# Kernel tuning notes

Measured on AMD Instinct MI355X. Metric: run time of the kernel, lower is better.

## Reference

```python
import jax, jax.numpy as jnp
import numpy as np

B, L, H, D = 2, 2048, 16, 64
E = H * D  # 1024

def setup_inputs() -> dict:
    key = jax.random.key(0)
    k1, k2, k3 = jax.random.split(key, 3)
    net_in = jax.random.normal(k1, (B, L, E), dtype=jnp.float32)
    # torch nn.Linear weights are [out_features, in_features]; scale like kaiming-uniform-ish
    W_qkv = jax.random.normal(k2, (3 * E, E), dtype=jnp.float32) * (1.0 / np.sqrt(E))
    W_out = jax.random.normal(k3, (E, E), dtype=jnp.float32) * (1.0 / np.sqrt(E))
    return {"net_in": net_in, "W_qkv": W_qkv, "W_out": W_out}

def reference(net_in, W_qkv, W_out):
    b, l, c = net_in.shape
    h, d = H, D
    # c_proj: x @ W_qkv.T -> (B, L, 3E), split into q, k, v
    qkv = jnp.einsum('blc,ec->ble', net_in, W_qkv)
    q, k, v = jnp.split(qkv, 3, axis=-1)
    # reshape to (B, H, L, D)
    q = q.reshape(b, l, h, d).transpose(0, 2, 1, 3)
    k = k.reshape(b, l, h, d).transpose(0, 2, 1, 3)
    v = v.reshape(b, l, h, d).transpose(0, 2, 1, 3)
    scale = 1.0 / np.sqrt(d).astype(np.float32)
    attn = jnp.einsum('bhqd,bhkd->bhqk', q, k) * scale  # (B, H, L, L)
    causal = jnp.tril(jnp.ones((l, l), dtype=bool))
    attn = jnp.where(causal[None, None, :, :], attn, -jnp.inf)
    attn = jax.nn.softmax(attn, axis=-1)
    out = jnp.einsum('bhqk,bhkd->bhqd', attn, v)  # (B, H, L, D)
    out = out.transpose(0, 2, 1, 3).reshape(b, l, c)
    return jnp.einsum('blc,ec->ble', out, W_out)
```

## Files before the change

### kernel.cpp

```cpp
#include <hip/hip_runtime.h>
#include <hip/hip_bf16.h>

#define LOG2E 1.44269504088896340736f

typedef __attribute__((ext_vector_type(8))) short s16x8;
typedef __attribute__((ext_vector_type(4))) short s16x4;
typedef __attribute__((ext_vector_type(2))) unsigned int u32x2;
typedef __attribute__((ext_vector_type(4))) float f32x4;

__device__ inline short f2bf(float f) {
  __hip_bfloat16 h = __float2bfloat16(f);
  union { __hip_bfloat16 h; short s; } u; u.h = h; return u.s;
}

__device__ inline void gl_lds16(const void* g, void* l) {
  __builtin_amdgcn_global_load_lds(
      (const __attribute__((address_space(1))) void*)g,
      (__attribute__((address_space(3))) void*)l, 16, 0, 0);
}

__global__ __launch_bounds__(256)
void cvt_all(const float* __restrict__ Wqkv, const float* __restrict__ Wout,
             const float* __restrict__ net,
             short* __restrict__ dWqkv, short* __restrict__ dWout,
             short* __restrict__ dnet) {
  int bid = blockIdx.x;
  const float* src; short* dst; int i;
  if (bid < 3072)      { src = Wqkv; dst = dWqkv; i = bid * 256 + threadIdx.x; }
  else if (bid < 4096) { src = Wout; dst = dWout; i = (bid - 3072) * 256 + threadIdx.x; }
  else                 { src = net;  dst = dnet;  i = (bid - 4096) * 256 + threadIdx.x; }
  f32x4 v = ((const f32x4*)src)[i];
  s16x4 o;
  o[0] = f2bf(v[0]); o[1] = f2bf(v[1]); o[2] = f2bf(v[2]); o[3] = f2bf(v[3]);
  ((s16x4*)dst)[i] = o;
}

template<int OUTF32, int VTRANS>
__global__ __launch_bounds__(256)
void gemm128(const short* __restrict__ A, int lda,
             const short* __restrict__ B,
             void* __restrict__ Cp, int ldc, int K) {
  int m0 = blockIdx.x * 128;
  int n0 = blockIdx.y * 128;
  int t = threadIdx.x;
  int w = t >> 6, lane = t & 63;
  int l16 = lane & 15, quad = lane >> 4;
  int wm = w >> 1, wn = w & 1;

  __shared__ __align__(16) short Bs[128 * 32];
  __shared__ __align__(16) short As[128 * 32];

  int scell = ((t & 3) ^ ((t >> 3) & 3)) * 8;
  const short* bsrc = B + (size_t)(n0 + (t >> 2)) * K + scell;
  const short* asrc = A + (size_t)(m0 + (t >> 2)) * lda + scell;
  int rcell = (quad ^ ((l16 >> 1) & 3)) * 8;

  f32x4 acc[4][4];
#pragma unroll
  for (int i = 0; i < 4; ++i)
#pragma unroll
    for (int j = 0; j < 4; ++j) acc[i][j] = (f32x4){0.f, 0.f, 0.f, 0.f};

  for (int k0 = 0; k0 < K; k0 += 32) {
    __syncthreads();
#pragma unroll
    for (int r = 0; r < 2; ++r)
      gl_lds16(asrc + k0 + (size_t)r * 64 * lda, (char*)As + r * 4096 + w * 1024);
#pragma unroll
    for (int r = 0; r < 2; ++r)
      gl_lds16(bsrc + k0 + (size_t)r * 64 * K, (char*)Bs + r * 4096 + w * 1024);
    __syncthreads();

    s16x8 af[4], bf[4];
#pragma unroll
    for (int i = 0; i < 4; ++i) {
      af[i] = *(const s16x8*)(As + (wm * 64 + i * 16 + l16) * 32 + rcell);
      bf[i] = *(const s16x8*)(Bs + (wn * 64 + i * 16 + l16) * 32 + rcell);
    }
#pragma unroll
    for (int i = 0; i < 4; ++i)
#pragma unroll
      for (int j = 0; j < 4; ++j)
        acc[i][j] = __builtin_amdgcn_mfma_f32_16x16x32_bf16(af[i], bf[j], acc[i][j], 0, 0, 0);
  }

  if (VTRANS && n0 >= 2048) {
    short* Cs = (short*)Cp;
#pragma unroll
    for (int i = 0; i < 4; ++i)
#pragma unroll
      for (int j = 0; j < 4; ++j) {
        int colg = n0 + wn * 64 + j * 16 + l16;
        int d = colg & 63;
        size_t dst = (size_t)(m0 + wm * 64 + d) * ldc + (colg - d) + i * 16 + quad * 4;
        s16x4 ob;
#pragma unroll
        for (int rr = 0; rr < 4; ++rr) ob[rr] = f2bf(acc[i][j][rr]);
        *(s16x4*)(Cs + dst) = ob;
      }
  } else {
#pragma unroll
    for (int i = 0; i < 4; ++i)
#pragma unroll
      for (int j = 0; j < 4; ++j)
#pragma unroll
        for (int rr = 0; rr < 4; ++rr) {
          size_t row = m0 + wm * 64 + i * 16 + quad * 4 + rr;
          size_t col = n0 + wn * 64 + j * 16 + l16;
          if (OUTF32) ((float*)Cp)[row * ldc + col] = acc[i][j][rr];
          else        ((short*)Cp)[row * ldc + col] = f2bf(acc[i][j][rr]);
        }
  }
}

__global__ __launch_bounds__(256)
void attn(short* __restrict__ qkv) {
  const int L = 2048, E3 = 3072, EO = 1024;
  int id = (int)(blockIdx.x + (blockIdx.y << 5));
  int xcd = id & 7;
  int s = id >> 3;
  int bh = xcd * 4 + (s & 3);
  int u = s >> 2;
  int vv = u & 15;
  int qidx = (u & 16) ? (31 - vv) : vv;
  int b = bh >> 4, h = bh & 15;
  int q0 = qidx * 64;
  int t = threadIdx.x;
  int wave = t >> 6, lane = t & 63;
  int l16 = lane & 15, quad = lane >> 4;
  int qw = q0 + wave * 16;
  const float SENT = -3.0e38f;
  const float SC = 0.125f * LOG2E;

  __shared__ __align__(16) short Ks[2][2][64][32];
  __shared__ __align__(16) short Vt[2][2][64][32];
  __shared__ __align__(16) short Pw[4][16 * 64];

  int rowbase = b * L;
  const short* qp = qkv + (size_t)(rowbase + qw + l16) * E3 + h * 64 + quad * 8;
  s16x8 qf[2];
#pragma unroll
  for (int c = 0; c < 2; ++c) {
    s16x8 raw = *(const s16x8*)(qp + c * 32);
#pragma unroll
    for (int j = 0; j < 8; ++j) {
      union { float f; int i; } u2; u2.i = ((int)(unsigned short)raw[j]) << 16;
      raw[j] = f2bf(u2.f * SC);
    }
    qf[c] = raw;
  }

  int scell = ((lane & 3) ^ ((lane >> 3) & 3)) * 8;
  const short* ksrc = qkv + (size_t)(rowbase + wave * 16 + (lane >> 2)) * E3 + EO
                      + h * 64 + scell;
  const short* vsrc = qkv + (size_t)(rowbase + wave * 16 + (lane >> 2)) * E3 + 2 * EO
                      + h * 64 + scell;
  int rcell = (quad ^ ((l16 >> 1) & 3)) * 8;
  int pbase = l16 * 64, pxor = l16 & 7;

  float l_acc = 0.f;
  f32x4 o[4];
#pragma unroll
  for (int j = 0; j < 4; ++j) o[j] = (f32x4){0.f, 0.f, 0.f, 0.f};

  int nkb = qidx + 1;

  gl_lds16(ksrc,      (char*)Ks + wave * 1024);
  gl_lds16(ksrc + 32, (char*)Ks + 4096 + wave * 1024);
  gl_lds16(vsrc,      (char*)Vt + wave * 1024);
  gl_lds16(vsrc + 32, (char*)Vt + 4096 + wave * 1024);

  for (int kb = 0; kb < nkb; ++kb) {
    int cur = kb & 1;
    __syncthreads();
    if (kb + 1 < nkb) {
      size_t koff = (size_t)((kb + 1) * 64) * E3;
      int nb = cur ^ 1;
      gl_lds16(ksrc + koff,      (char*)Ks + nb * 8192 + wave * 1024);
      gl_lds16(ksrc + koff + 32, (char*)Ks + nb * 8192 + 4096 + wave * 1024);
      gl_lds16(vsrc + koff,      (char*)Vt + nb * 8192 + wave * 1024);
      gl_lds16(vsrc + koff + 32, (char*)Vt + nb * 8192 + 4096 + wave * 1024);
    }

    int mtile = (qw - kb * 64) >> 4;

    f32x4 sf[4];
#pragma unroll
    for (int st = 0; st < 4; ++st) {
      if (st <= mtile) {
        s16x8 kf0 = *(const s16x8*)(&Ks[cur][0][st * 16 + l16][0] + rcell);
        s16x8 kf1 = *(const s16x8*)(&Ks[cur][1][st * 16 + l16][0] + rcell);
        f32x4 tt = (f32x4){0.f, 0.f, 0.f, 0.f};
        tt = __builtin_amdgcn_mfma_f32_16x16x32_bf16(kf0, qf[0], tt, 0, 0, 0);
        tt = __builtin_amdgcn_mfma_f32_16x16x32_bf16(kf1, qf[1], tt, 0, 0, 0);
        sf[st] = tt;
      }
    }
    if (mtile < 4) {
#pragma unroll
      for (int st = 0; st < 4; ++st) {
        if (st == mtile) {
#pragma unroll
          for (int r = 0; r < 4; ++r)
            if (quad * 4 + r > l16) sf[st][r] = SENT;
        } else if (st > mtile) {
          sf[st] = (f32x4){SENT, SENT, SENT, SENT};
        }
      }
    }

#pragma unroll
    for (int st = 0; st < 4; ++st)
#pragma unroll
      for (int r = 0; r < 4; ++r) {
        float p = __builtin_amdgcn_exp2f(sf[st][r]);
        sf[st][r] = p;
        l_acc += p;
      }

#pragma unroll
    for (int st = 0; st < 4; ++st) {
      unsigned u0 = __float_as_uint(sf[st][0]) + 0x8000u;
      unsigned u1 = __float_as_uint(sf[st][1]) + 0x8000u;
      unsigned u2 = __float_as_uint(sf[st][2]) + 0x8000u;
      unsigned u3 = __float_as_uint(sf[st][3]) + 0x8000u;
      u32x2 d;
      d[0] = __builtin_amdgcn_perm(u1, u0, 0x07060302u);
      d[1] = __builtin_amdgcn_perm(u3, u2, 0x07060302u);
      int cw = (st * 2 + (quad >> 1)) ^ pxor;
      *(u32x2*)(&Pw[wave][pbase + cw * 8 + (quad & 1) * 4]) = d;
    }
    asm volatile("s_waitcnt lgkmcnt(0)" ::: "memory");
#pragma unroll
    for (int kc = 0; kc < 2; ++kc) {
      s16x8 pf = *(const s16x8*)(&Pw[wave][pbase + (((kc * 4 + quad) ^ pxor) * 8)]);
#pragma unroll
      for (int j = 0; j < 4; ++j) {
        s16x8 vf = *(const s16x8*)(&Vt[cur][kc][j * 16 + l16][0] + rcell);
        o[j] = __builtin_amdgcn_mfma_f32_16x16x32_bf16(vf, pf, o[j], 0, 0, 0);
      }
    }
  }

  l_acc += __shfl_xor(l_acc, 16);
  l_acc += __shfl_xor(l_acc, 32);
  float inv = 1.f / l_acc;
  size_t obase = (size_t)(rowbase + qw + l16) * E3 + h * 64;
#pragma unroll
  for (int j = 0; j < 4; ++j) {
    s16x4 ob;
#pragma unroll
    for (int r = 0; r < 4; ++r) ob[r] = f2bf(o[j][r] * inv);
    *(s16x4*)(qkv + obase + j * 16 + quad * 4) = ob;
  }
}

extern "C" void kernel_launch(void* const* d_in, const int* in_sizes, int n_in,
                              void* d_out, int out_size, void* d_ws, size_t ws_size,
                              hipStream_t stream) {
  const float* net_in = (const float*)d_in[0];
  const float* W_qkv  = (const float*)d_in[1];
  const float* W_out  = (const float*)d_in[2];

  short* Wqkvb = (short*)d_ws;
  short* Woutb = Wqkvb + (size_t)3072 * 1024;
  short* qkv   = Woutb + (size_t)1024 * 1024;
  short* netb  = (short*)d_out;

  cvt_all<<<8192, 256, 0, stream>>>(W_qkv, W_out, net_in, Wqkvb, Woutb, netb);

  gemm128<0, 1><<<dim3(32, 24), 256, 0, stream>>>(netb, 1024, Wqkvb, qkv, 3072, 1024);
  attn<<<dim3(32, 32), 256, 0, stream>>>(qkv);
  gemm128<1, 0><<<dim3(32, 8), 256, 0, stream>>>(qkv, 3072, Woutb, d_out, 1024, 1024);
}
```

Measured before the change: 185.8 us.

## Process two 64-row query tiles per attention block to reuse K/V loads

Each attention workgroup now handles 128 query rows, as two groups of 16 rows per wave, instead of 64. Every K/V tile staged in LDS therefore feeds twice as many MFMAs, and the grid is halved. The query-pair mapping is changed so causal work stays balanced. The cost is more registers (two accumulator sets, launch bounds of 256 with 2 blocks), fewer blocks to fill the CUs, and some wasted masked work on the first tile's diagonal blocks.

```diff
diff --git a/kernel.cpp b/kernel.cpp
--- a/kernel.cpp
+++ b/kernel.cpp
@@ -113,7 +113,7 @@
   }
 }
 
-__global__ __launch_bounds__(256)
+__global__ __launch_bounds__(256, 2)
 void attn(short* __restrict__ qkv) {
   const int L = 2048, E3 = 3072, EO = 1024;
   int id = (int)(blockIdx.x + (blockIdx.y << 5));
@@ -121,33 +121,36 @@
   int s = id >> 3;
   int bh = xcd * 4 + (s & 3);
   int u = s >> 2;
-  int vv = u & 15;
-  int qidx = (u & 16) ? (31 - vv) : vv;
+  int qp = (u < 8) ? u : 23 - u;
   int b = bh >> 4, h = bh & 15;
-  int q0 = qidx * 64;
+  int q0 = qp * 128;
   int t = threadIdx.x;
   int wave = t >> 6, lane = t & 63;
   int l16 = lane & 15, quad = lane >> 4;
-  int qw = q0 + wave * 16;
+  int qw0 = q0 + wave * 16;
+  int qw1 = qw0 + 64;
   const float SENT = -3.0e38f;
   const float SC = 0.125f * LOG2E;
 
   __shared__ __align__(16) short Ks[2][2][64][32];
   __shared__ __align__(16) short Vt[2][2][64][32];
-  __shared__ __align__(16) short Pw[4][16 * 64];
+  __shared__ __align__(16) short Pw[4][2][16 * 64];
 
   int rowbase = b * L;
-  const short* qp = qkv + (size_t)(rowbase + qw + l16) * E3 + h * 64 + quad * 8;
-  s16x8 qf[2];
-#pragma unroll
-  for (int c = 0; c < 2; ++c) {
-    s16x8 raw = *(const s16x8*)(qp + c * 32);
-#pragma unroll
-    for (int j = 0; j < 8; ++j) {
-      union { float f; int i; } u2; u2.i = ((int)(unsigned short)raw[j]) << 16;
-      raw[j] = f2bf(u2.f * SC);
-    }
-    qf[c] = raw;
+  s16x8 qf[2][2];
+#pragma unroll
+  for (int g = 0; g < 2; ++g) {
+    const short* qp_ptr = qkv + (size_t)(rowbase + qw0 + g * 64 + l16) * E3 + h * 64 + quad * 8;
+#pragma unroll
+    for (int c = 0; c < 2; ++c) {
+      s16x8 raw = *(const s16x8*)(qp_ptr + c * 32);
+#pragma unroll
+      for (int j = 0; j < 8; ++j) {
+        union { float f; int i; } u2; u2.i = ((int)(unsigned short)raw[j]) << 16;
+        raw[j] = f2bf(u2.f * SC);
+      }
+      qf[g][c] = raw;
+    }
   }
 
   int scell = ((lane & 3) ^ ((lane >> 3) & 3)) * 8;
@@ -158,12 +161,12 @@
   int rcell = (quad ^ ((l16 >> 1) & 3)) * 8;
   int pbase = l16 * 64, pxor = l16 & 7;
 
-  float l_acc = 0.f;
-  f32x4 o[4];
-#pragma unroll
-  for (int j = 0; j < 4; ++j) o[j] = (f32x4){0.f, 0.f, 0.f, 0.f};
-
-  int nkb = qidx + 1;
+  float l0 = 0.f, l1 = 0.f;
+  f32x4 o0[4], o1[4];
+#pragma unroll
+  for (int j = 0; j < 4; ++j) { o0[j] = (f32x4){0.f,0.f,0.f,0.f}; o1[j] = (f32x4){0.f,0.f,0.f,0.f}; }
+
+  int nkb = 2 * qp + 2;
 
   gl_lds16(ksrc,      (char*)Ks + wave * 1024);
   gl_lds16(ksrc + 32, (char*)Ks + 4096 + wave * 1024);
@@ -182,76 +185,117 @@
       gl_lds16(vsrc + koff + 32, (char*)Vt + nb * 8192 + 4096 + wave * 1024);
     }
 
-    int mtile = (qw - kb * 64) >> 4;
-
-    f32x4 sf[4];
+    int mt0 = (qw0 - kb * 64) >> 4;
+    int mt1 = mt0 + 4;
+
+    f32x4 sf0[4], sf1[4];
 #pragma unroll
     for (int st = 0; st < 4; ++st) {
-      if (st <= mtile) {
+      if (st <= mt1) {
         s16x8 kf0 = *(const s16x8*)(&Ks[cur][0][st * 16 + l16][0] + rcell);
         s16x8 kf1 = *(const s16x8*)(&Ks[cur][1][st * 16 + l16][0] + rcell);
+        if (st <= mt0) {
+          f32x4 tt = (f32x4){0.f, 0.f, 0.f, 0.f};
+          tt = __builtin_amdgcn_mfma_f32_16x16x32_bf16(kf0, qf[0][0], tt, 0, 0, 0);
+          tt = __builtin_amdgcn_mfma_f32_16x16x32_bf16(kf1, qf[0][1], tt, 0, 0, 0);
+          sf0[st] = tt;
+        }
         f32x4 tt = (f32x4){0.f, 0.f, 0.f, 0.f};
-        tt = __builtin_amdgcn_mfma_f32_16x16x32_bf16(kf0, qf[0], tt, 0, 0, 0);
-        tt = __builtin_amdgcn_mfma_f32_16x16x32_bf16(kf1, qf[1], tt, 0, 0, 0);
-        sf[st] = tt;
-      }
-    }
-    if (mtile < 4) {
+        tt = __builtin_amdgcn_mfma_f32_16x16x32_bf16(kf0, qf[1][0], tt, 0, 0, 0);
+        tt = __builtin_amdgcn_mfma_f32_16x16x32_bf16(kf1, qf[1][1], tt, 0, 0, 0);
+        sf1[st] = tt;
+      }
+    }
+    if (mt0 < 4) {
 #pragma unroll
       for (int st = 0; st < 4; ++st) {
-        if (st == mtile) {
+        if (st == mt0) {
 #pragma unroll
           for (int r = 0; r < 4; ++r)
-            if (quad * 4 + r > l16) sf[st][r] = SENT;
-        } else if (st > mtile) {
-          sf[st] = (f32x4){SENT, SENT, SENT, SENT};
+            if (quad * 4 + r > l16) sf0[st][r] = SENT;
+        } else if (st > mt0) {
+          sf0[st] = (f32x4){SENT, SENT, SENT, SENT};
         }
       }
     }
+    if (mt1 < 4) {
+#pragma unroll
+      for (int st = 0; st < 4; ++st) {
+        if (st == mt1) {
+#pragma unroll
+          for (int r = 0; r < 4; ++r)
+            if (quad * 4 + r > l16) sf1[st][r] = SENT;
+        } else if (st > mt1) {
+          sf1[st] = (f32x4){SENT, SENT, SENT, SENT};
+        }
+      }
+    }
 
 #pragma unroll
     for (int st = 0; st < 4; ++st)
 #pragma unroll
       for (int r = 0; r < 4; ++r) {
-        float p = __builtin_amdgcn_exp2f(sf[st][r]);
-        sf[st][r] = p;
-        l_acc += p;
+        float p0 = __builtin_amdgcn_exp2f(sf0[st][r]);
+        sf0[st][r] = p0; l0 += p0;
+        float p1 = __builtin_amdgcn_exp2f(sf1[st][r]);
+        sf1[st][r] = p1; l1 += p1;
       }
 
 #pragma unroll
     for (int st = 0; st < 4; ++st) {
-      unsigned u0 = __float_as_uint(sf[st][0]) + 0x8000u;
-      unsigned u1 = __float_as_uint(sf[st][1]) + 0x8000u;
-      unsigned u2 = __float_as_uint(sf[st][2]) + 0x8000u;
-      unsigned u3 = __float_as_uint(sf[st][3]) + 0x8000u;
-      u32x2 d;
-      d[0] = __builtin_amdgcn_perm(u1, u0, 0x07060302u);
-      d[1] = __builtin_amdgcn_perm(u3, u2, 0x07060302u);
       int cw = (st * 2 + (quad >> 1)) ^ pxor;
-      *(u32x2*)(&Pw[wave][pbase + cw * 8 + (quad & 1) * 4]) = d;
+      {
+        unsigned a0 = __float_as_uint(sf0[st][0]) + 0x8000u;
+        unsigned a1 = __float_as_uint(sf0[st][1]) + 0x8000u;
+        unsigned a2 = __float_as_uint(sf0[st][2]) + 0x8000u;
+        unsigned a3 = __float_as_uint(sf0[st][3]) + 0x8000u;
+        u32x2 d;
+        d[0] = __builtin_amdgcn_perm(a1, a0, 0x07060302u);
+        d[1] = __builtin_amdgcn_perm(a3, a2, 0x07060302u);
+        *(u32x2*)(&Pw[wave][0][pbase + cw * 8 + (quad & 1) * 4]) = d;
+      }
+      {
+        unsigned a0 = __float_as_uint(sf1[st][0]) + 0x8000u;
+        unsigned a1 = __float_as_uint(sf1[st][1]) + 0x8000u;
+        unsigned a2 = __float_as_uint(sf1[st][2]) + 0x8000u;
+        unsigned a3 = __float_as_uint(sf1[st][3]) + 0x8000u;
+        u32x2 d;
+        d[0] = __builtin_amdgcn_perm(a1, a0, 0x07060302u);
+        d[1] = __builtin_amdgcn_perm(a3, a2, 0x07060302u);
+        *(u32x2*)(&Pw[wave][1][pbase + cw * 8 + (quad & 1) * 4]) = d;
+      }
     }
     asm volatile("s_waitcnt lgkmcnt(0)" ::: "memory");
 #pragma unroll
     for (int kc = 0; kc < 2; ++kc) {
-      s16x8 pf = *(const s16x8*)(&Pw[wave][pbase + (((kc * 4 + quad) ^ pxor) * 8)]);
+      s16x8 pf0 = *(const s16x8*)(&Pw[wave][0][pbase + (((kc * 4 + quad) ^ pxor) * 8)]);
+      s16x8 pf1 = *(const s16x8*)(&Pw[wave][1][pbase + (((kc * 4 + quad) ^ pxor) * 8)]);
 #pragma unroll
       for (int j = 0; j < 4; ++j) {
         s16x8 vf = *(const s16x8*)(&Vt[cur][kc][j * 16 + l16][0] + rcell);
-        o[j] = __builtin_amdgcn_mfma_f32_16x16x32_bf16(vf, pf, o[j], 0, 0, 0);
-      }
-    }
-  }
-
-  l_acc += __shfl_xor(l_acc, 16);
-  l_acc += __shfl_xor(l_acc, 32);
-  float inv = 1.f / l_acc;
-  size_t obase = (size_t)(rowbase + qw + l16) * E3 + h * 64;
+        o0[j] = __builtin_amdgcn_mfma_f32_16x16x32_bf16(vf, pf0, o0[j], 0, 0, 0);
+        o1[j] = __builtin_amdgcn_mfma_f32_16x16x32_bf16(vf, pf1, o1[j], 0, 0, 0);
+      }
+    }
+  }
+
+  l0 += __shfl_xor(l0, 16);
+  l0 += __shfl_xor(l0, 32);
+  l1 += __shfl_xor(l1, 16);
+  l1 += __shfl_xor(l1, 32);
+  float inv0 = 1.f / l0, inv1 = 1.f / l1;
+  size_t ob0 = (size_t)(rowbase + qw0 + l16) * E3 + h * 64;
+  size_t ob1 = (size_t)(rowbase + qw1 + l16) * E3 + h * 64;
 #pragma unroll
   for (int j = 0; j < 4; ++j) {
-    s16x4 ob;
-#pragma unroll
-    for (int r = 0; r < 4; ++r) ob[r] = f2bf(o[j][r] * inv);
-    *(s16x4*)(qkv + obase + j * 16 + quad * 4) = ob;
+    s16x4 w0, w1;
+#pragma unroll
+    for (int r = 0; r < 4; ++r) {
+      w0[r] = f2bf(o0[j][r] * inv0);
+      w1[r] = f2bf(o1[j][r] * inv1);
+    }
+    *(s16x4*)(qkv + ob0 + j * 16 + quad * 4) = w0;
+    *(s16x4*)(qkv + ob1 + j * 16 + quad * 4) = w1;
   }
 }
 
@@ -270,6 +314,6 @@
   cvt_all<<<8192, 256, 0, stream>>>(W_qkv, W_out, net_in, Wqkvb, Woutb, netb);
 
   gemm128<0, 1><<<dim3(32, 24), 256, 0, stream>>>(netb, 1024, Wqkvb, qkv, 3072, 1024);
-  attn<<<dim3(32, 32), 256, 0, stream>>>(qkv);
+  attn<<<dim3(32, 16), 256, 0, stream>>>(qkv);
   gemm128<1, 0><<<dim3(32, 8), 256, 0, stream>>>(qkv, 3072, Woutb, d_out, 1024, 1024);
 }
```

New measurement: 200.6 us. 8.0% more time.

## Switch attention to 32x32 MFMA with in-register P via permlane swap and key split

Applied to the files above, without the earlier changes.

Reworks the attention kernel to use 32x32x16 bf16 MFMAs, with waves split into 2 query halves × 2 key halves. The P tile now moves between lane halves with permlane32_swap instead of a round trip through LDS, and the two key-half partial outputs are combined through shared memory at the end. This is meant to remove the LDS traffic and waitcnt stall for P, cut the MFMA instruction count, and let fully masked key halves be skipped. The cost is a final cross-wave reduction with two barriers, and half the waves sit idle during the output write.

```diff
diff --git a/kernel.cpp b/kernel.cpp
--- a/kernel.cpp
+++ b/kernel.cpp
@@ -7,6 +7,7 @@
 typedef __attribute__((ext_vector_type(4))) short s16x4;
 typedef __attribute__((ext_vector_type(2))) unsigned int u32x2;
 typedef __attribute__((ext_vector_type(4))) float f32x4;
+typedef __attribute__((ext_vector_type(16))) float f32x16;
 
 __device__ inline short f2bf(float f) {
   __hip_bfloat16 h = __float2bfloat16(f);
@@ -113,7 +114,7 @@
   }
 }
 
-__global__ __launch_bounds__(256)
+__global__ __launch_bounds__(256, 4)
 void attn(short* __restrict__ qkv) {
   const int L = 2048, E3 = 3072, EO = 1024;
   int id = (int)(blockIdx.x + (blockIdx.y << 5));
@@ -127,27 +128,31 @@
   int q0 = qidx * 64;
   int t = threadIdx.x;
   int wave = t >> 6, lane = t & 63;
-  int l16 = lane & 15, quad = lane >> 4;
-  int qw = q0 + wave * 16;
+  int qh = wave >> 1, kh = wave & 1;
+  int l31 = lane & 31, hsel = lane >> 5;
+  int khi4 = hsel * 4;
+  int key = (lane >> 1) & 3;
   const float SENT = -3.0e38f;
   const float SC = 0.125f * LOG2E;
 
   __shared__ __align__(16) short Ks[2][2][64][32];
   __shared__ __align__(16) short Vt[2][2][64][32];
-  __shared__ __align__(16) short Pw[4][16 * 64];
 
   int rowbase = b * L;
-  const short* qp = qkv + (size_t)(rowbase + qw + l16) * E3 + h * 64 + quad * 8;
-  s16x8 qf[2];
-#pragma unroll
-  for (int c = 0; c < 2; ++c) {
-    s16x8 raw = *(const s16x8*)(qp + c * 32);
-#pragma unroll
-    for (int j = 0; j < 8; ++j) {
-      union { float f; int i; } u2; u2.i = ((int)(unsigned short)raw[j]) << 16;
-      raw[j] = f2bf(u2.f * SC);
-    }
-    qf[c] = raw;
+
+  s16x8 qf[4];
+  {
+    const short* qp = qkv + (size_t)(rowbase + q0 + qh * 32 + l31) * E3 + h * 64 + hsel * 8;
+#pragma unroll
+    for (int e = 0; e < 4; ++e) {
+      s16x8 raw = *(const s16x8*)(qp + e * 16);
+#pragma unroll
+      for (int j = 0; j < 8; ++j) {
+        union { float f; int i; } u2; u2.i = ((int)(unsigned short)raw[j]) << 16;
+        raw[j] = f2bf(u2.f * SC);
+      }
+      qf[e] = raw;
+    }
   }
 
   int scell = ((lane & 3) ^ ((lane >> 3) & 3)) * 8;
@@ -155,13 +160,10 @@
                       + h * 64 + scell;
   const short* vsrc = qkv + (size_t)(rowbase + wave * 16 + (lane >> 2)) * E3 + 2 * EO
                       + h * 64 + scell;
-  int rcell = (quad ^ ((l16 >> 1) & 3)) * 8;
-  int pbase = l16 * 64, pxor = l16 & 7;
 
   float l_acc = 0.f;
-  f32x4 o[4];
-#pragma unroll
-  for (int j = 0; j < 4; ++j) o[j] = (f32x4){0.f, 0.f, 0.f, 0.f};
+  f32x16 o0 = (f32x16){0.f,0.f,0.f,0.f,0.f,0.f,0.f,0.f,0.f,0.f,0.f,0.f,0.f,0.f,0.f,0.f};
+  f32x16 o1 = o0;
 
   int nkb = qidx + 1;
 
@@ -182,76 +184,91 @@
       gl_lds16(vsrc + koff + 32, (char*)Vt + nb * 8192 + 4096 + wave * 1024);
     }
 
-    int mtile = (qw - kb * 64) >> 4;
-
-    f32x4 sf[4];
-#pragma unroll
-    for (int st = 0; st < 4; ++st) {
-      if (st <= mtile) {
-        s16x8 kf0 = *(const s16x8*)(&Ks[cur][0][st * 16 + l16][0] + rcell);
-        s16x8 kf1 = *(const s16x8*)(&Ks[cur][1][st * 16 + l16][0] + rcell);
-        f32x4 tt = (f32x4){0.f, 0.f, 0.f, 0.f};
-        tt = __builtin_amdgcn_mfma_f32_16x16x32_bf16(kf0, qf[0], tt, 0, 0, 0);
-        tt = __builtin_amdgcn_mfma_f32_16x16x32_bf16(kf1, qf[1], tt, 0, 0, 0);
-        sf[st] = tt;
-      }
-    }
-    if (mtile < 4) {
-#pragma unroll
-      for (int st = 0; st < 4; ++st) {
-        if (st == mtile) {
-#pragma unroll
-          for (int r = 0; r < 4; ++r)
-            if (quad * 4 + r > l16) sf[st][r] = SENT;
-        } else if (st > mtile) {
-          sf[st] = (f32x4){SENT, SENT, SENT, SENT};
+    int rel = (q0 + qh * 32) - (kb * 64 + kh * 32);
+    if (rel > -32) {
+      int krow = kh * 32 + l31;
+      s16x8 kf0 = *(const s16x8*)(&Ks[cur][0][krow][((0 + hsel) ^ key) * 8]);
+      s16x8 kf1 = *(const s16x8*)(&Ks[cur][0][krow][((2 + hsel) ^ key) * 8]);
+      s16x8 kf2 = *(const s16x8*)(&Ks[cur][1][krow][((0 + hsel) ^ key) * 8]);
+      s16x8 kf3 = *(const s16x8*)(&Ks[cur][1][krow][((2 + hsel) ^ key) * 8]);
+      s16x8 vf00 = *(const s16x8*)(&Vt[cur][kh][ 0 + l31][((0 + hsel) ^ key) * 8]);
+      s16x8 vf01 = *(const s16x8*)(&Vt[cur][kh][32 + l31][((0 + hsel) ^ key) * 8]);
+      s16x8 vf10 = *(const s16x8*)(&Vt[cur][kh][ 0 + l31][((2 + hsel) ^ key) * 8]);
+      s16x8 vf11 = *(const s16x8*)(&Vt[cur][kh][32 + l31][((2 + hsel) ^ key) * 8]);
+
+      f32x16 sf = (f32x16){0.f,0.f,0.f,0.f,0.f,0.f,0.f,0.f,0.f,0.f,0.f,0.f,0.f,0.f,0.f,0.f};
+      sf = __builtin_amdgcn_mfma_f32_32x32x16_bf16(kf0, qf[0], sf, 0, 0, 0);
+      sf = __builtin_amdgcn_mfma_f32_32x32x16_bf16(kf1, qf[1], sf, 0, 0, 0);
+      sf = __builtin_amdgcn_mfma_f32_32x32x16_bf16(kf2, qf[2], sf, 0, 0, 0);
+      sf = __builtin_amdgcn_mfma_f32_32x32x16_bf16(kf3, qf[3], sf, 0, 0, 0);
+
+      if (rel < 31) {
+        int thr = rel + l31 - khi4;
+#pragma unroll
+        for (int r = 0; r < 16; ++r) {
+          const int base_k = (r & 3) + 8 * (r >> 2);
+          if (base_k > thr) sf[r] = SENT;
         }
       }
-    }
-
-#pragma unroll
-    for (int st = 0; st < 4; ++st)
-#pragma unroll
-      for (int r = 0; r < 4; ++r) {
-        float p = __builtin_amdgcn_exp2f(sf[st][r]);
-        sf[st][r] = p;
-        l_acc += p;
-      }
-
-#pragma unroll
-    for (int st = 0; st < 4; ++st) {
-      unsigned u0 = __float_as_uint(sf[st][0]) + 0x8000u;
-      unsigned u1 = __float_as_uint(sf[st][1]) + 0x8000u;
-      unsigned u2 = __float_as_uint(sf[st][2]) + 0x8000u;
-      unsigned u3 = __float_as_uint(sf[st][3]) + 0x8000u;
-      u32x2 d;
-      d[0] = __builtin_amdgcn_perm(u1, u0, 0x07060302u);
-      d[1] = __builtin_amdgcn_perm(u3, u2, 0x07060302u);
-      int cw = (st * 2 + (quad >> 1)) ^ pxor;
-      *(u32x2*)(&Pw[wave][pbase + cw * 8 + (quad & 1) * 4]) = d;
-    }
-    asm volatile("s_waitcnt lgkmcnt(0)" ::: "memory");
-#pragma unroll
-    for (int kc = 0; kc < 2; ++kc) {
-      s16x8 pf = *(const s16x8*)(&Pw[wave][pbase + (((kc * 4 + quad) ^ pxor) * 8)]);
-#pragma unroll
-      for (int j = 0; j < 4; ++j) {
-        s16x8 vf = *(const s16x8*)(&Vt[cur][kc][j * 16 + l16][0] + rcell);
-        o[j] = __builtin_amdgcn_mfma_f32_16x16x32_bf16(vf, pf, o[j], 0, 0, 0);
-      }
-    }
-  }
-
-  l_acc += __shfl_xor(l_acc, 16);
+
+      float pv[16];
+#pragma unroll
+      for (int r = 0; r < 16; ++r) {
+        pv[r] = __builtin_amdgcn_exp2f(sf[r]);
+        l_acc += pv[r];
+      }
+
+#define PKW(lo, hi) __builtin_amdgcn_perm(__float_as_uint(hi) + 0x8000u, \
+                                          __float_as_uint(lo) + 0x8000u, 0x07060302u)
+      unsigned A0 = PKW(pv[0],  pv[1]),  A1 = PKW(pv[2],  pv[3]);
+      unsigned B0 = PKW(pv[4],  pv[5]),  B1 = PKW(pv[6],  pv[7]);
+      unsigned C0 = PKW(pv[8],  pv[9]),  C1 = PKW(pv[10], pv[11]);
+      unsigned D0 = PKW(pv[12], pv[13]), D1 = PKW(pv[14], pv[15]);
+#undef PKW
+      u32x2 sw0 = __builtin_amdgcn_permlane32_swap(A0, B0, false, false);
+      u32x2 sw1 = __builtin_amdgcn_permlane32_swap(A1, B1, false, false);
+      u32x2 sw2 = __builtin_amdgcn_permlane32_swap(C0, D0, false, false);
+      u32x2 sw3 = __builtin_amdgcn_permlane32_swap(C1, D1, false, false);
+      union { s16x8 v; unsigned u[4]; } P0, P1;
+      P0.u[0] = sw0[0]; P0.u[1] = sw1[0]; P0.u[2] = sw0[1]; P0.u[3] = sw1[1];
+      P1.u[0] = sw2[0]; P1.u[1] = sw3[0]; P1.u[2] = sw2[1]; P1.u[3] = sw3[1];
+
+      o0 = __builtin_amdgcn_mfma_f32_32x32x16_bf16(vf00, P0.v, o0, 0, 0, 0);
+      o0 = __builtin_amdgcn_mfma_f32_32x32x16_bf16(vf10, P1.v, o0, 0, 0, 0);
+      o1 = __builtin_amdgcn_mfma_f32_32x32x16_bf16(vf01, P0.v, o1, 0, 0, 0);
+      o1 = __builtin_amdgcn_mfma_f32_32x32x16_bf16(vf11, P1.v, o1, 0, 0, 0);
+    }
+  }
+
   l_acc += __shfl_xor(l_acc, 32);
-  float inv = 1.f / l_acc;
-  size_t obase = (size_t)(rowbase + qw + l16) * E3 + h * 64;
-#pragma unroll
-  for (int j = 0; j < 4; ++j) {
-    s16x4 ob;
-#pragma unroll
-    for (int r = 0; r < 4; ++r) ob[r] = f2bf(o[j][r] * inv);
-    *(s16x4*)(qkv + obase + j * 16 + quad * 4) = ob;
+  __syncthreads();
+  float* fs = (float*)&Ks[0][0][0][0];
+  float* lb = (float*)&Vt[0][0][0][0];
+  if (kh) {
+#pragma unroll
+    for (int r = 0; r < 16; ++r) {
+      fs[qh * 2048 + r * 64 + lane] = o0[r];
+      fs[qh * 2048 + (16 + r) * 64 + lane] = o1[r];
+    }
+    if (lane < 32) lb[qh * 32 + lane] = l_acc;
+  }
+  __syncthreads();
+  if (!kh) {
+    float inv = 1.f / (l_acc + lb[qh * 32 + l31]);
+    size_t obase = (size_t)(rowbase + q0 + qh * 32 + l31) * E3 + h * 64;
+    int fb = qh * 2048;
+#pragma unroll
+    for (int g = 0; g < 4; ++g) {
+      s16x4 w0, w1;
+#pragma unroll
+      for (int rr = 0; rr < 4; ++rr) {
+        int r = g * 4 + rr;
+        w0[rr] = f2bf((o0[r] + fs[fb + r * 64 + lane]) * inv);
+        w1[rr] = f2bf((o1[r] + fs[fb + (16 + r) * 64 + lane]) * inv);
+      }
+      *(s16x4*)(qkv + obase + g * 8 + khi4) = w0;
+      *(s16x4*)(qkv + obase + 32 + g * 8 + khi4) = w1;
+    }
   }
 }
 
```

New measurement: 177.1 us. 1.05x faster.
